# Performance work log

Hardware: AMD Instinct MI355X
Metric: run time of the kernel (lower is better)

Reference implementation:

```python
import jax, jax.numpy as jnp
import numpy as np

B, N, CIN, H, W = 4, 512, 128, 376, 376
WIN_H, WIN_W = 4, 7
OUT_C = WIN_H * WIN_W  # num_parts * num_class (num_class=1)
SPATIAL_SCALE = 1.0    # 1 / FEATMAP_STRIDE
GRID_OFF = (0.0, 0.0)
BN_EPS = 1e-3


def setup_inputs() -> dict:
    key = jax.random.key(0)
    k1, k2, k3, k4, k5, k6 = jax.random.split(key, 6)
    feat = jax.random.normal(k1, (B, CIN, H, W), jnp.float32)
    w1 = jax.random.normal(k2, (CIN, CIN, 3, 3), jnp.float32) * (1.0 / np.sqrt(CIN * 9))
    gamma = jax.random.uniform(k3, (CIN,), jnp.float32, 0.5, 1.5)
    beta = jax.random.normal(k4, (CIN,), jnp.float32) * 0.1
    run_mean = jnp.zeros((CIN,), jnp.float32)
    run_var = jnp.ones((CIN,), jnp.float32)
    w2 = jax.random.normal(k5, (OUT_C, CIN), jnp.float32) * (1.0 / np.sqrt(CIN))
    # boxes: (x, y, w, l, rot) in feature-map coords, i.e. box[:, [0,1,3,4,6]]
    u = jax.random.uniform(k6, (B, N, 5), jnp.float32)
    bx = u[..., 0] * (W - 1)
    by = u[..., 1] * (H - 1)
    bw = u[..., 2] * 15.0 + 5.0
    bl = u[..., 3] * 15.0 + 5.0
    br = (u[..., 4] * 2.0 - 1.0) * np.pi
    boxes5 = jnp.stack([bx, by, bw, bl, br], axis=-1)
    return {"feat": feat, "w1": w1, "gamma": gamma, "beta": beta,
            "run_mean": run_mean, "run_var": run_var, "w2": w2, "boxes5": boxes5}


def _grid_points(boxes5):
    # rotated sampling grid, matching gen_sample_grid (row-major over WIN_H x WIN_W)
    xg, yg, wg, lg, rg = [boxes5[..., i] for i in range(5)]  # each [B, N]
    cos = jnp.cos(rg)[..., None, None]
    sin = jnp.sin(rg)[..., None, None]
    xx = jnp.linspace(-0.5, 0.5, WIN_H, dtype=boxes5.dtype)[:, None] * wg[..., None, None]  # [B,N,WIN_H,1]
    yy = jnp.linspace(-0.5, 0.5, WIN_W, dtype=boxes5.dtype)[None, :] * lg[..., None, None]  # [B,N,1,WIN_W]
    px = (xx * cos + yy * sin + xg[..., None, None] + GRID_OFF[0]) * SPATIAL_SCALE  # [B,N,WIN_H,WIN_W]
    py = (yy * cos - xx * sin + yg[..., None, None] + GRID_OFF[1]) * SPATIAL_SCALE
    return px.reshape(B, N, OUT_C), py.reshape(B, N, OUT_C)


def _forward(feat, w1, gamma, beta, run_mean, run_var, w2, boxes5):
    # convs_1: 3x3 conv (pad=1, no bias) + BatchNorm (eval, running stats) + ReLU
    x = jax.lax.conv_general_dilated(feat, w1, (1, 1), 'SAME',
                                     dimension_numbers=('NCHW', 'OIHW', 'NCHW'))
    scale = (gamma * jax.lax.rsqrt(run_var + BN_EPS))[:, None, None]
    shift = (beta - run_mean * gamma * jax.lax.rsqrt(run_var + BN_EPS))[:, None, None]
    x = jax.nn.relu(x * scale + shift)
    # convs_conf: 1x1 conv, no bias -> confi_im [B, OUT_C, H, W]
    confi_im = jnp.einsum('bchw,oc->bohw', x, w2)

    px, py = _grid_points(boxes5)  # [B, N, OUT_C] each; part k samples channel k
    # grid_sample normalization in source: g = 2*s/(dim-1) - 1, then default
    # align_corners=False maps pixel = ((g+1)*dim - 1)/2 = s*dim/(dim-1) - 0.5
    fx = px * (W / (W - 1.0)) - 0.5
    fy = py * (H / (H - 1.0)) - 0.5
    x0 = jnp.floor(fx)
    y0 = jnp.floor(fy)
    wx = fx - x0  # bilinear weights
    wy = fy - y0

    bidx = jnp.arange(B)[:, None, None]
    kidx = jnp.arange(OUT_C)[None, None, :]

    def gather(xf, yf):
        # zero padding outside the image (grid_sample padding_mode='zeros')
        valid = (xf >= 0) & (xf <= W - 1) & (yf >= 0) & (yf <= H - 1)
        xc = jnp.clip(xf, 0, W - 1).astype(jnp.int32)
        yc = jnp.clip(yf, 0, H - 1).astype(jnp.int32)
        v = confi_im[bidx, kidx, yc, xc]
        return jnp.where(valid, v, jnp.zeros_like(v))

    v00 = gather(x0, y0)
    v10 = gather(x0 + 1, y0)
    v01 = gather(x0, y0 + 1)
    v11 = gather(x0 + 1, y0 + 1)
    samp = (v00 * (1 - wx) * (1 - wy) + v10 * wx * (1 - wy)
            + v01 * (1 - wx) * wy + v11 * wx * wy)      # [B, N, OUT_C]
    conf = jnp.mean(samp, axis=-1)                       # mean over the 28 parts
    return jax.nn.sigmoid(conf)                          # batch_cls_preds, [B, N]


def reference(feat, w1, gamma, beta, run_mean, run_var, w2, boxes5):
    return _forward(feat, w1, gamma, beta, run_mean, run_var, w2, boxes5)
```

## Files before the change

kernel.cpp:

```cpp
#include <hip/hip_runtime.h>
#include <math.h>

#define NB   4
#define NBOX 512
#define CI   128
#define HH   376
#define WW   376
#define OC   28
#define HW   (HH * WW)

typedef short short8  __attribute__((ext_vector_type(8)));
typedef __bf16 bf16x8 __attribute__((ext_vector_type(8)));
typedef float f32x16  __attribute__((ext_vector_type(16)));
typedef unsigned uint4v __attribute__((ext_vector_type(4)));

typedef const __attribute__((address_space(1))) void gas_void;
typedef __attribute__((address_space(3))) void las_void;

__device__ inline unsigned short f2bf(float f) {
    unsigned u = __builtin_bit_cast(unsigned, f);
    u = u + 0x7fffu + ((u >> 16) & 1u);
    return (unsigned short)(u >> 16);
}

__device__ inline unsigned cvtpk_bf16(float lo, float hi) {
    unsigned r;
    asm("v_cvt_pk_bf16_f32 %0, %1, %2" : "=v"(r) : "v"(lo), "v"(hi));
    return r;
}

__device__ inline f32x16 mfma32(short8 a, short8 b, f32x16 c) {
    return __builtin_amdgcn_mfma_f32_32x32x16_bf16(
        __builtin_bit_cast(bf16x8, a), __builtin_bit_cast(bf16x8, b), c, 0, 0, 0);
}

__global__ void __launch_bounds__(256)
prep_kernel(const float* __restrict__ w1, const float* __restrict__ gamma,
            const float* __restrict__ beta, const float* __restrict__ rmean,
            const float* __restrict__ rvar, const float* __restrict__ w2,
            unsigned short* __restrict__ w1p, unsigned short* __restrict__ w2pB,
            float* __restrict__ bnsc, float* __restrict__ bnsh,
            unsigned short* __restrict__ zbuf)
{
    int idx = blockIdx.x * 256 + threadIdx.x;
    if (idx < 8 * 128 * 9 * 16) {
        int e    = idx & 7;
        int sp   = (idx >> 3) & 1;
        int t9   = idx >> 4;
        int tap  = t9 % 9;
        int t2   = t9 / 9;
        int co   = t2 & 127;
        int chnk = t2 >> 7;
        int s    = sp ^ ((co >> 2) & 1);
        int ci   = chnk * 16 + s * 8 + e;
        w1p[idx] = f2bf(w1[((size_t)co * CI + ci) * 9 + tap]);
    }
    if (idx < 32 * 128) {
        int o = idx >> 7, k = idx & 127;
        w2pB[idx] = (o < OC) ? f2bf(w2[o * CI + k]) : (unsigned short)0;
    }
    if (idx < CI) {
        float rs = rsqrtf(rvar[idx] + 1e-3f);
        bnsc[idx] = gamma[idx] * rs;
        bnsh[idx] = beta[idx] - rmean[idx] * gamma[idx] * rs;
    }
    if (idx < 128) zbuf[idx] = 0;
}

__global__ void __launch_bounds__(256)
prepass_kernel(const float* __restrict__ feat, unsigned short* __restrict__ featp)
{
    __shared__ unsigned short xl[64 * 136];
    const int t  = threadIdx.x;
    const int bb = blockIdx.x;
    const int b  = bb / 2209;
    const int s0 = (bb - b * 2209) * 64;

    const int pxq = t & 15;
    const int cib = t >> 4;
#pragma unroll
    for (int it = 0; it < 8; ++it) {
        int ci = it * 16 + cib;
        float4 v = *(const float4*)(feat + ((size_t)(b * CI + ci)) * HW + s0 + pxq * 4);
#pragma unroll
        for (int j = 0; j < 4; ++j)
            xl[(pxq * 4 + j) * 136 + ci] = f2bf((&v.x)[j]);
    }
    __syncthreads();
#pragma unroll
    for (int it = 0; it < 4; ++it) {
        int n  = it * 256 + t;
        int px = n >> 4, cs = n & 15;
        short8 v = *(const short8*)(xl + px * 136 + cs * 8);
        *(short8*)(featp + ((size_t)b * HW + s0 + px) * 128 + cs * 8) = v;
    }
}

__global__ void __launch_bounds__(256, 2)
conv_mfma(const unsigned short* __restrict__ featp,
          const unsigned short* __restrict__ w1p,
          const float* __restrict__ bnsc, const float* __restrict__ bnsh,
          const unsigned short* __restrict__ w2pB,
          const unsigned short* __restrict__ zbuf,
          float* __restrict__ confi)
{
    __shared__ unsigned short sm[24064];
    unsigned short* featl = sm;
    unsigned short* wl    = sm + 5632;

    const int tid  = threadIdx.x;
    const int w    = tid >> 6;
    const int lane = tid & 63;
    const int l31  = lane & 31;
    const int h    = lane >> 5;
    const int x0   = blockIdx.x * 16;
    const int y0   = blockIdx.y * 16;
    const int b    = blockIdx.z;

    const unsigned short* fsrc[3];
#pragma unroll
    for (int j = 0; j < 3; ++j) {
        int i  = w + 4 * j;
        int L  = i * 64 + lane;
        int px = L >> 1, s = L & 1;
        int r  = px / 18, cc = px - r * 18;
        int gy = y0 + r - 1, gx = x0 + cc - 1;
        bool ok = (px < 324) && ((unsigned)gy < HH) && ((unsigned)gx < WW);
        int sp = s ^ ((px >> 2) & 1);
        fsrc[j] = ok ? (featp + (((size_t)b * HW + (size_t)gy * WW + gx) * 128) + sp * 8)
                     : (zbuf + sp * 8);
    }

    int pxb[2];
#pragma unroll
    for (int pf = 0; pf < 2; ++pf)
        pxb[pf] = (w * 4 + pf * 2 + (l31 >> 4)) * 18 + (l31 & 15);
    int slA[4];
#pragma unroll
    for (int nf = 0; nf < 4; ++nf) {
        int co = nf * 32 + l31;
        slA[nf] = co * 18 + (h ^ ((co >> 2) & 1));
    }

    f32x16 acc[4][2];
#pragma unroll
    for (int nf = 0; nf < 4; ++nf)
#pragma unroll
        for (int pf = 0; pf < 2; ++pf)
#pragma unroll
            for (int e = 0; e < 16; ++e) acc[nf][pf][e] = 0.f;

    for (int chunk = 0; chunk < 8; ++chunk) {
        __syncthreads();
#pragma unroll
        for (int j = 0; j < 3; ++j) {
            int i = w + 4 * j;
            if (i < 11)
                __builtin_amdgcn_global_load_lds(
                    (gas_void*)(fsrc[j] + chunk * 16),
                    (las_void*)(featl + i * 512), 16, 0, 0);
        }
#pragma unroll
        for (int j = 0; j < 9; ++j) {
            int i = w * 9 + j;
            __builtin_amdgcn_global_load_lds(
                (gas_void*)(w1p + (size_t)chunk * 18432 + (i * 64 + lane) * 8),
                (las_void*)(wl + i * 512), 16, 0, 0);
        }
        __syncthreads();

#pragma unroll
        for (int tap = 0; tap < 9; ++tap) {
            const int dy = tap / 3, dx = tap - 3 * (tap / 3);
            short8 bfv[2], afv[4];
#pragma unroll
            for (int pf = 0; pf < 2; ++pf) {
                int pxl = pxb[pf] + dy * 18 + dx;
                int sl  = h ^ ((pxl >> 2) & 1);
                bfv[pf] = *(const short8*)(featl + pxl * 16 + sl * 8);
            }
#pragma unroll
            for (int nf = 0; nf < 4; ++nf)
                afv[nf] = *(const short8*)(wl + slA[nf] * 8 + tap * 16);
#pragma unroll
            for (int nf = 0; nf < 4; ++nf)
#pragma unroll
                for (int pf = 0; pf < 2; ++pf)
                    acc[nf][pf] = mfma32(afv[nf], bfv[pf], acc[nf][pf]);
        }
    }

#pragma unroll
    for (int nf = 0; nf < 4; ++nf)
#pragma unroll
        for (int q = 0; q < 4; ++q) {
            float4 s4 = *(const float4*)(bnsc + nf * 32 + q * 8 + 4 * h);
            float4 t4 = *(const float4*)(bnsh + nf * 32 + q * 8 + 4 * h);
#pragma unroll
            for (int r = 0; r < 4; ++r)
#pragma unroll
                for (int pf = 0; pf < 2; ++pf)
                    acc[nf][pf][q * 4 + r] =
                        fmaxf(acc[nf][pf][q * 4 + r] * (&s4.x)[r] + (&t4.x)[r], 0.f);
        }

#pragma unroll
    for (int pf = 0; pf < 2; ++pf) {
        f32x16 o2;
#pragma unroll
        for (int e = 0; e < 16; ++e) o2[e] = 0.f;
#pragma unroll
        for (int nf = 0; nf < 4; ++nf) {
#pragma unroll
            for (int half = 0; half < 2; ++half) {
                const int qa = half * 2, qb = half * 2 + 1;
                unsigned A0 = cvtpk_bf16(acc[nf][pf][qa * 4 + 0], acc[nf][pf][qa * 4 + 1]);
                unsigned A1 = cvtpk_bf16(acc[nf][pf][qa * 4 + 2], acc[nf][pf][qa * 4 + 3]);
                unsigned B0 = cvtpk_bf16(acc[nf][pf][qb * 4 + 0], acc[nf][pf][qb * 4 + 1]);
                unsigned B1 = cvtpk_bf16(acc[nf][pf][qb * 4 + 2], acc[nf][pf][qb * 4 + 3]);
                unsigned sA0 = (unsigned)__shfl_xor((int)A0, 32);
                unsigned sA1 = (unsigned)__shfl_xor((int)A1, 32);
                unsigned sB0 = (unsigned)__shfl_xor((int)B0, 32);
                unsigned sB1 = (unsigned)__shfl_xor((int)B1, 32);
                uint4v uv;
                uv[0] = h ? sB0 : A0;
                uv[1] = h ? sB1 : A1;
                uv[2] = h ? B0  : sA0;
                uv[3] = h ? B1  : sA1;
                short8 a2 = __builtin_bit_cast(short8, uv);
                int ks = nf * 2 + half;
                short8 wfv = *(const short8*)(w2pB + l31 * 128 + ks * 16 + h * 8);
                o2 = mfma32(a2, wfv, o2);
            }
        }
#pragma unroll
        for (int reg = 0; reg < 16; ++reg) {
            int row = (reg & 3) + 8 * (reg >> 2) + 4 * h;
            int pxl = w * 64 + pf * 32 + row;
            int y = y0 + (pxl >> 4), x = x0 + (pxl & 15);
            if (l31 < OC && x < WW && y < HH)
                confi[(((size_t)b * HH + y) * WW + x) * OC + l31] = o2[reg];
        }
    }
}

__global__ void __launch_bounds__(256)
sample_kernel(const float* __restrict__ confi, const float* __restrict__ boxes,
              float* __restrict__ out)
{
    const int tid = threadIdx.x;
    const int lb  = tid >> 5;
    const int k   = tid & 31;
    const int box = blockIdx.x * 8 + lb;
    const int b   = box >> 9;
    const int n   = box & 511;

    const float* b5 = boxes + ((size_t)b * NBOX + n) * 5;
    float xg = b5[0], yg = b5[1], wg = b5[2], lg = b5[3], rg = b5[4];
    float cr = cosf(rg), sr = sinf(rg);

    float samp = 0.f;
    if (k < OC) {
        int i = k / 7, j = k - 7 * i;
        float xx = (-0.5f + (float)i * (1.0f / 3.0f)) * wg;
        float yy = (-0.5f + (float)j * (1.0f / 6.0f)) * lg;
        float px = xx * cr + yy * sr + xg;
        float py = yy * cr - xx * sr + yg;
        float fx = px * ((float)WW / (float)(WW - 1)) - 0.5f;
        float fy = py * ((float)HH / (float)(HH - 1)) - 0.5f;
        float x0f = floorf(fx), y0f = floorf(fy);
        float wx = fx - x0f, wy = fy - y0f;
        int xi = (int)x0f, yi = (int)y0f;

        float v00 = 0.f, v10 = 0.f, v01 = 0.f, v11 = 0.f;
        bool okx0 = (xi >= 0)     && (xi <= WW - 1);
        bool okx1 = (xi + 1 >= 0) && (xi + 1 <= WW - 1);
        bool oky0 = (yi >= 0)     && (yi <= HH - 1);
        bool oky1 = (yi + 1 >= 0) && (yi + 1 <= HH - 1);
        if (okx0 && oky0) v00 = confi[(((size_t)b * HH + yi)     * WW + xi)     * OC + k];
        if (okx1 && oky0) v10 = confi[(((size_t)b * HH + yi)     * WW + xi + 1) * OC + k];
        if (okx0 && oky1) v01 = confi[(((size_t)b * HH + yi + 1) * WW + xi)     * OC + k];
        if (okx1 && oky1) v11 = confi[(((size_t)b * HH + yi + 1) * WW + xi + 1) * OC + k];
        samp = v00 * (1.f - wx) * (1.f - wy) + v10 * wx * (1.f - wy)
             + v01 * (1.f - wx) * wy         + v11 * wx * wy;
    }
#pragma unroll
    for (int m = 16; m >= 1; m >>= 1) samp += __shfl_xor(samp, m, 64);

    if (k == 0) {
        float conf = samp * (1.0f / (float)OC);
        out[box] = 1.f / (1.f + expf(-conf));
    }
}

extern "C" void kernel_launch(void* const* d_in, const int* in_sizes, int n_in,
                              void* d_out, int out_size, void* d_ws, size_t ws_size,
                              hipStream_t stream)
{
    const float* feat  = (const float*)d_in[0];
    const float* w1    = (const float*)d_in[1];
    const float* gamma = (const float*)d_in[2];
    const float* beta  = (const float*)d_in[3];
    const float* rmean = (const float*)d_in[4];
    const float* rvar  = (const float*)d_in[5];
    const float* w2    = (const float*)d_in[6];
    const float* boxes = (const float*)d_in[7];
    float* out = (float*)d_out;

    char* ws = (char*)d_ws;
    float*          confi = (float*)ws;
    unsigned short* featp = (unsigned short*)(ws + 63336448);
    unsigned short* w1p   = (unsigned short*)(ws + 208105472);
    unsigned short* w2pB  = (unsigned short*)(ws + 208400384);
    float*          bnsc  = (float*)(ws + 208408576);
    float*          bnsh  = (float*)(ws + 208409088);
    unsigned short* zbuf  = (unsigned short*)(ws + 208409600);

    prep_kernel<<<576, 256, 0, stream>>>(w1, gamma, beta, rmean, rvar, w2,
                                         w1p, w2pB, bnsc, bnsh, zbuf);

    prepass_kernel<<<NB * 2209, 256, 0, stream>>>(feat, featp);

    dim3 grid(24, 24, NB);
    conv_mfma<<<grid, 256, 0, stream>>>(featp, w1p, bnsc, bnsh, w2pB, zbuf, confi);

    sample_kernel<<<NB * NBOX / 8, 256, 0, stream>>>(confi, boxes, out);
}
```

Baseline: 262.8 us.

## Double-buffer LDS staging in conv MFMA kernel to overlap loads with compute

```diff
diff --git a/kernel.cpp b/kernel.cpp
--- a/kernel.cpp
+++ b/kernel.cpp
@@ -96,7 +96,28 @@
     }
 }
 
-__global__ void __launch_bounds__(256, 2)
+#define STAGE(P, CH)                                                            \
+    {                                                                           \
+        unsigned short* fd = sm + (P) * 5632;                                   \
+        unsigned short* wd = sm + 11264 + (P) * 18432;                          \
+        _Pragma("unroll")                                                       \
+        for (int j = 0; j < 3; ++j) {                                           \
+            int i = w + 4 * j;                                                  \
+            if (i < 11)                                                         \
+                __builtin_amdgcn_global_load_lds(                               \
+                    (gas_void*)(fsrc[j] + (CH) * 16),                           \
+                    (las_void*)(fd + i * 512), 16, 0, 0);                       \
+        }                                                                       \
+        _Pragma("unroll")                                                       \
+        for (int j = 0; j < 9; ++j) {                                           \
+            int i = w * 9 + j;                                                  \
+            __builtin_amdgcn_global_load_lds(                                   \
+                (gas_void*)(w1p + (size_t)(CH) * 18432 + (i * 64 + lane) * 8),  \
+                (las_void*)(wd + i * 512), 16, 0, 0);                           \
+        }                                                                       \
+    }
+
+__global__ void __launch_bounds__(256, 1)
 conv_mfma(const unsigned short* __restrict__ featp,
           const unsigned short* __restrict__ w1p,
           const float* __restrict__ bnsc, const float* __restrict__ bnsh,
@@ -104,9 +125,7 @@
           const unsigned short* __restrict__ zbuf,
           float* __restrict__ confi)
 {
-    __shared__ unsigned short sm[24064];
-    unsigned short* featl = sm;
-    unsigned short* wl    = sm + 5632;
+    extern __shared__ unsigned short sm[];
 
     const int tid  = threadIdx.x;
     const int w    = tid >> 6;
@@ -150,24 +169,14 @@
 #pragma unroll
             for (int e = 0; e < 16; ++e) acc[nf][pf][e] = 0.f;
 
+    STAGE(0, 0)
+    __syncthreads();
+
     for (int chunk = 0; chunk < 8; ++chunk) {
-        __syncthreads();
-#pragma unroll
-        for (int j = 0; j < 3; ++j) {
-            int i = w + 4 * j;
-            if (i < 11)
-                __builtin_amdgcn_global_load_lds(
-                    (gas_void*)(fsrc[j] + chunk * 16),
-                    (las_void*)(featl + i * 512), 16, 0, 0);
-        }
-#pragma unroll
-        for (int j = 0; j < 9; ++j) {
-            int i = w * 9 + j;
-            __builtin_amdgcn_global_load_lds(
-                (gas_void*)(w1p + (size_t)chunk * 18432 + (i * 64 + lane) * 8),
-                (las_void*)(wl + i * 512), 16, 0, 0);
-        }
-        __syncthreads();
+        if (chunk < 7) STAGE((chunk + 1) & 1, chunk + 1)
+
+        const unsigned short* featl = sm + (chunk & 1) * 5632;
+        const unsigned short* wl    = sm + 11264 + (chunk & 1) * 18432;
 
 #pragma unroll
         for (int tap = 0; tap < 9; ++tap) {
@@ -188,6 +197,7 @@
                 for (int pf = 0; pf < 2; ++pf)
                     acc[nf][pf] = mfma32(afv[nf], bfv[pf], acc[nf][pf]);
         }
+        __syncthreads();
     }
 
 #pragma unroll
@@ -321,8 +331,10 @@
 
     prepass_kernel<<<NB * 2209, 256, 0, stream>>>(feat, featp);
 
+    hipFuncSetAttribute((const void*)conv_mfma,
+                        hipFuncAttributeMaxDynamicSharedMemorySize, 96256);
     dim3 grid(24, 24, NB);
-    conv_mfma<<<grid, 256, 0, stream>>>(featp, w1p, bnsc, bnsh, w2pB, zbuf, confi);
+    conv_mfma<<<grid, 256, 96256, stream>>>(featp, w1p, bnsc, bnsh, w2pB, zbuf, confi);
 
     sample_kernel<<<NB * NBOX / 8, 256, 0, stream>>>(confi, boxes, out);
 }
```

After: 279.5 us. +6.3%, slower.

## Read conv input tiles directly from global memory instead of staging in LDS

Applied to the files above, without the earlier changes.

```diff
diff --git a/kernel.cpp b/kernel.cpp
--- a/kernel.cpp
+++ b/kernel.cpp
@@ -8,6 +8,7 @@
 #define WW   376
 #define OC   28
 #define HW   (HH * WW)
+#define ZOFF 145073152u
 
 typedef short short8  __attribute__((ext_vector_type(8)));
 typedef __bf16 bf16x8 __attribute__((ext_vector_type(8)));
@@ -101,12 +102,9 @@
           const unsigned short* __restrict__ w1p,
           const float* __restrict__ bnsc, const float* __restrict__ bnsh,
           const unsigned short* __restrict__ w2pB,
-          const unsigned short* __restrict__ zbuf,
           float* __restrict__ confi)
 {
-    __shared__ unsigned short sm[24064];
-    unsigned short* featl = sm;
-    unsigned short* wl    = sm + 5632;
+    __shared__ unsigned short wl[18432];
 
     const int tid  = threadIdx.x;
     const int w    = tid >> 6;
@@ -116,31 +114,33 @@
     const int x0   = blockIdx.x * 16;
     const int y0   = blockIdx.y * 16;
     const int b    = blockIdx.z;
-
-    const unsigned short* fsrc[3];
-#pragma unroll
-    for (int j = 0; j < 3; ++j) {
-        int i  = w + 4 * j;
-        int L  = i * 64 + lane;
-        int px = L >> 1, s = L & 1;
-        int r  = px / 18, cc = px - r * 18;
-        int gy = y0 + r - 1, gx = x0 + cc - 1;
-        bool ok = (px < 324) && ((unsigned)gy < HH) && ((unsigned)gx < WW);
-        int sp = s ^ ((px >> 2) & 1);
-        fsrc[j] = ok ? (featp + (((size_t)b * HW + (size_t)gy * WW + gx) * 128) + sp * 8)
-                     : (zbuf + sp * 8);
-    }
-
-    int pxb[2];
-#pragma unroll
-    for (int pf = 0; pf < 2; ++pf)
-        pxb[pf] = (w * 4 + pf * 2 + (l31 >> 4)) * 18 + (l31 & 15);
-    int slA[4];
-#pragma unroll
-    for (int nf = 0; nf < 4; ++nf) {
-        int co = nf * 32 + l31;
-        slA[nf] = co * 18 + (h ^ ((co >> 2) & 1));
-    }
+    const char* fpB = (const char*)featp;
+
+    unsigned off0[9], off1[9];
+    {
+        const int lc = l31 & 15;
+#pragma unroll
+        for (int tap = 0; tap < 9; ++tap) {
+            const int dy = tap / 3, dx = tap - 3 * (tap / 3);
+#pragma unroll
+            for (int pf = 0; pf < 2; ++pf) {
+                int lr = w * 4 + pf * 2 + (l31 >> 4);
+                int gy = y0 + lr + dy - 1;
+                int gx = x0 + lc + dx - 1;
+                bool ok = ((unsigned)gy < HH) && ((unsigned)gx < WW);
+                unsigned o = ok
+                    ? (unsigned)(((size_t)b * HW + (size_t)gy * WW + gx) * 256 + h * 16)
+                    : (ZOFF + (unsigned)(h * 16));
+                if (pf == 0) off0[tap] = o; else off1[tap] = o;
+            }
+        }
+    }
+
+    const int sw   = h ^ ((l31 >> 2) & 1);
+    const int slA0 = (0 * 32 + l31) * 18 + sw;
+    const int slA1 = (1 * 32 + l31) * 18 + sw;
+    const int slA2 = (2 * 32 + l31) * 18 + sw;
+    const int slA3 = (3 * 32 + l31) * 18 + sw;
 
     f32x16 acc[4][2];
 #pragma unroll
@@ -152,14 +152,6 @@
 
     for (int chunk = 0; chunk < 8; ++chunk) {
         __syncthreads();
-#pragma unroll
-        for (int j = 0; j < 3; ++j) {
-            int i = w + 4 * j;
-            if (i < 11)
-                __builtin_amdgcn_global_load_lds(
-                    (gas_void*)(fsrc[j] + chunk * 16),
-                    (las_void*)(featl + i * 512), 16, 0, 0);
-        }
 #pragma unroll
         for (int j = 0; j < 9; ++j) {
             int i = w * 9 + j;
@@ -171,23 +163,24 @@
 
 #pragma unroll
         for (int tap = 0; tap < 9; ++tap) {
-            const int dy = tap / 3, dx = tap - 3 * (tap / 3);
-            short8 bfv[2], afv[4];
-#pragma unroll
-            for (int pf = 0; pf < 2; ++pf) {
-                int pxl = pxb[pf] + dy * 18 + dx;
-                int sl  = h ^ ((pxl >> 2) & 1);
-                bfv[pf] = *(const short8*)(featl + pxl * 16 + sl * 8);
-            }
-#pragma unroll
-            for (int nf = 0; nf < 4; ++nf)
-                afv[nf] = *(const short8*)(wl + slA[nf] * 8 + tap * 16);
-#pragma unroll
-            for (int nf = 0; nf < 4; ++nf)
-#pragma unroll
-                for (int pf = 0; pf < 2; ++pf)
-                    acc[nf][pf] = mfma32(afv[nf], bfv[pf], acc[nf][pf]);
-        }
+            short8 b0 = *(const short8*)(fpB + off0[tap]);
+            short8 b1 = *(const short8*)(fpB + off1[tap]);
+            short8 a0 = *(const short8*)(wl + slA0 * 8 + tap * 16);
+            short8 a1 = *(const short8*)(wl + slA1 * 8 + tap * 16);
+            short8 a2 = *(const short8*)(wl + slA2 * 8 + tap * 16);
+            short8 a3 = *(const short8*)(wl + slA3 * 8 + tap * 16);
+            acc[0][0] = mfma32(a0, b0, acc[0][0]);
+            acc[0][1] = mfma32(a0, b1, acc[0][1]);
+            acc[1][0] = mfma32(a1, b0, acc[1][0]);
+            acc[1][1] = mfma32(a1, b1, acc[1][1]);
+            acc[2][0] = mfma32(a2, b0, acc[2][0]);
+            acc[2][1] = mfma32(a2, b1, acc[2][1]);
+            acc[3][0] = mfma32(a3, b0, acc[3][0]);
+            acc[3][1] = mfma32(a3, b1, acc[3][1]);
+        }
+
+#pragma unroll
+        for (int t2 = 0; t2 < 9; ++t2) { off0[t2] += 32; off1[t2] += 32; }
     }
 
 #pragma unroll
@@ -322,7 +315,7 @@
     prepass_kernel<<<NB * 2209, 256, 0, stream>>>(feat, featp);
 
     dim3 grid(24, 24, NB);
-    conv_mfma<<<grid, 256, 0, stream>>>(featp, w1p, bnsc, bnsh, w2pB, zbuf, confi);
+    conv_mfma<<<grid, 256, 0, stream>>>(featp, w1p, bnsc, bnsh, w2pB, confi);
 
     sample_kernel<<<NB * NBOX / 8, 256, 0, stream>>>(confi, boxes, out);
 }
```

New measurement: 343.4 us. 1.31x slower.

## Split per-chunk weight staging into two tap phases to shrink LDS footprint

Applied to the files above, without the earlier changes.

```diff
diff --git a/kernel.cpp b/kernel.cpp
--- a/kernel.cpp
+++ b/kernel.cpp
@@ -43,14 +43,14 @@
             unsigned short* __restrict__ zbuf)
 {
     int idx = blockIdx.x * 256 + threadIdx.x;
-    if (idx < 8 * 128 * 9 * 16) {
+    if (idx < 8 * 9 * 128 * 16) {
         int e    = idx & 7;
         int sp   = (idx >> 3) & 1;
-        int t9   = idx >> 4;
-        int tap  = t9 % 9;
-        int t2   = t9 / 9;
+        int t2   = idx >> 4;
         int co   = t2 & 127;
-        int chnk = t2 >> 7;
+        int t3   = t2 >> 7;
+        int tap  = t3 % 9;
+        int chnk = t3 / 9;
         int s    = sp ^ ((co >> 2) & 1);
         int ci   = chnk * 16 + s * 8 + e;
         w1p[idx] = f2bf(w1[((size_t)co * CI + ci) * 9 + tap]);
@@ -104,7 +104,7 @@
           const unsigned short* __restrict__ zbuf,
           float* __restrict__ confi)
 {
-    __shared__ unsigned short sm[24064];
+    __shared__ unsigned short sm[15872];
     unsigned short* featl = sm;
     unsigned short* wl    = sm + 5632;
 
@@ -135,12 +135,11 @@
 #pragma unroll
     for (int pf = 0; pf < 2; ++pf)
         pxb[pf] = (w * 4 + pf * 2 + (l31 >> 4)) * 18 + (l31 & 15);
-    int slA[4];
-#pragma unroll
-    for (int nf = 0; nf < 4; ++nf) {
-        int co = nf * 32 + l31;
-        slA[nf] = co * 18 + (h ^ ((co >> 2) & 1));
-    }
+    const int sw = h ^ ((l31 >> 2) & 1);
+    int coff[4];
+#pragma unroll
+    for (int nf = 0; nf < 4; ++nf)
+        coff[nf] = (nf * 32 + l31) * 16 + sw * 8;
 
     f32x16 acc[4][2];
 #pragma unroll
@@ -151,6 +150,7 @@
             for (int e = 0; e < 16; ++e) acc[nf][pf][e] = 0.f;
 
     for (int chunk = 0; chunk < 8; ++chunk) {
+        const unsigned short* wsrc = w1p + (size_t)chunk * 18432;
         __syncthreads();
 #pragma unroll
         for (int j = 0; j < 3; ++j) {
@@ -161,16 +161,16 @@
                     (las_void*)(featl + i * 512), 16, 0, 0);
         }
 #pragma unroll
-        for (int j = 0; j < 9; ++j) {
-            int i = w * 9 + j;
+        for (int j = 0; j < 5; ++j) {
+            int i = w + 4 * j;
             __builtin_amdgcn_global_load_lds(
-                (gas_void*)(w1p + (size_t)chunk * 18432 + (i * 64 + lane) * 8),
+                (gas_void*)(wsrc + i * 512 + lane * 8),
                 (las_void*)(wl + i * 512), 16, 0, 0);
         }
         __syncthreads();
 
 #pragma unroll
-        for (int tap = 0; tap < 9; ++tap) {
+        for (int tap = 0; tap < 5; ++tap) {
             const int dy = tap / 3, dx = tap - 3 * (tap / 3);
             short8 bfv[2], afv[4];
 #pragma unroll
@@ -181,7 +181,37 @@
             }
 #pragma unroll
             for (int nf = 0; nf < 4; ++nf)
-                afv[nf] = *(const short8*)(wl + slA[nf] * 8 + tap * 16);
+                afv[nf] = *(const short8*)(wl + tap * 2048 + coff[nf]);
+#pragma unroll
+            for (int nf = 0; nf < 4; ++nf)
+#pragma unroll
+                for (int pf = 0; pf < 2; ++pf)
+                    acc[nf][pf] = mfma32(afv[nf], bfv[pf], acc[nf][pf]);
+        }
+
+        __syncthreads();
+#pragma unroll
+        for (int j = 0; j < 4; ++j) {
+            int i = w + 4 * j;
+            __builtin_amdgcn_global_load_lds(
+                (gas_void*)(wsrc + 10240 + i * 512 + lane * 8),
+                (las_void*)(wl + i * 512), 16, 0, 0);
+        }
+        __syncthreads();
+
+#pragma unroll
+        for (int tap = 5; tap < 9; ++tap) {
+            const int dy = tap / 3, dx = tap - 3 * (tap / 3);
+            short8 bfv[2], afv[4];
+#pragma unroll
+            for (int pf = 0; pf < 2; ++pf) {
+                int pxl = pxb[pf] + dy * 18 + dx;
+                int sl  = h ^ ((pxl >> 2) & 1);
+                bfv[pf] = *(const short8*)(featl + pxl * 16 + sl * 8);
+            }
+#pragma unroll
+            for (int nf = 0; nf < 4; ++nf)
+                afv[nf] = *(const short8*)(wl + (tap - 5) * 2048 + coff[nf]);
 #pragma unroll
             for (int nf = 0; nf < 4; ++nf)
 #pragma unroll
```

Result: slower. 272.4 us (+3.7%).
